# Kernel optimization log

Measured on AMD Instinct MI355X. Metric: run time of the kernel, lower is better.

The kernel has to match this reference:

```python
import jax, jax.numpy as jnp
import numpy as np

D = 512
B, S1, S2 = 8, 2048, 2048


def setup_inputs() -> dict:
    key = jax.random.key(0)
    ks = jax.random.split(key, 8)
    s = 1.0 / np.sqrt(D)
    return {
        "x1": jax.random.normal(ks[0], (B, S1, D), dtype=jnp.float32),
        "x2": jax.random.normal(ks[1], (B, S2, D), dtype=jnp.float32),
        "Wq": jax.random.normal(ks[2], (D, D), dtype=jnp.float32) * s,
        "bq": jnp.zeros((D,), dtype=jnp.float32),
        "Wk": jax.random.normal(ks[3], (D, D), dtype=jnp.float32) * s,
        "bk": jnp.zeros((D,), dtype=jnp.float32),
        "Wv": jax.random.normal(ks[4], (D, D), dtype=jnp.float32) * s,
        "bv": jnp.zeros((D,), dtype=jnp.float32),
    }


def reference(x1, x2, Wq, bq, Wk, bk, Wv, bv):
    # q,k,v projections (torch Linear: x @ W^T + b)
    q = jnp.einsum("bsd,ed->bse", x1, Wq) + bq  # [B,S1,D]
    k = jnp.einsum("btd,ed->bte", x2, Wk) + bk  # [B,S2,D]
    v = jnp.einsum("btd,ed->bte", x2, Wv) + bv  # [B,S2,D]
    # NOTE: source scales by input_dim (D), not sqrt(D)
    scores = jnp.einsum("bse,bte->bst", q, k) / D  # [B,S1,S2]
    attn = jax.nn.softmax(scores, axis=-1)
    return jnp.einsum("bst,bte->bse", attn, v)  # [B,S1,D]
```

## Files before the change

### kernel.cpp

```cpp
#include <hip/hip_runtime.h>

using u16 = unsigned short;
using u32 = unsigned int;
using s16x8 = __attribute__((ext_vector_type(8))) short;
using bf16x8 = __attribute__((ext_vector_type(8))) __bf16;
using f32x4 = __attribute__((ext_vector_type(4))) float;

__device__ inline u16 f2bf(float f) {
  u32 u = __float_as_uint(f);
  u = (u + 0x7FFFu + ((u >> 16) & 1u)) >> 16;
  return (u16)u;
}

__device__ inline f32x4 mfma16(s16x8 a, s16x8 b, f32x4 c) {
  return __builtin_amdgcn_mfma_f32_16x16x32_bf16(
      __builtin_bit_cast(bf16x8, a), __builtin_bit_cast(bf16x8, b), c, 0, 0, 0);
}

__device__ inline void load_lds16(const void* g, void* l) {
  __builtin_amdgcn_global_load_lds(
      (const __attribute__((address_space(1))) void*)g,
      (__attribute__((address_space(3))) void*)l, 16, 0, 0);
}

__global__ __launch_bounds__(256) void cast_x12(
    const float* __restrict__ x1, const float* __restrict__ x2,
    u16* __restrict__ o1, u16* __restrict__ o2) {
  const float* in = blockIdx.y ? x2 : x1;
  u16* out = blockIdx.y ? o2 : o1;
  int i = (blockIdx.x * 256 + threadIdx.x) * 4;
  float4 f = *(const float4*)(in + i);
  ushort4 o;
  o.x = f2bf(f.x); o.y = f2bf(f.y); o.z = f2bf(f.z); o.w = f2bf(f.w);
  *(ushort4*)(out + i) = o;
}

__global__ __launch_bounds__(256) void cast_w3z(
    const float* __restrict__ a, const float* __restrict__ b,
    const float* __restrict__ c, u16* __restrict__ oa, u16* __restrict__ ob,
    u16* __restrict__ oc, float* __restrict__ lbuf) {
  if (blockIdx.y == 3) {
    if (blockIdx.x < 64) lbuf[blockIdx.x * 256 + threadIdx.x] = 0.0f;
    return;
  }
  const float* in = blockIdx.y == 0 ? a : (blockIdx.y == 1 ? b : c);
  u16* out = blockIdx.y == 0 ? oa : (blockIdx.y == 1 ? ob : oc);
  int i = (blockIdx.x * 256 + threadIdx.x) * 4;
  float4 f = *(const float4*)(in + i);
  ushort4 o;
  o.x = f2bf(f.x); o.y = f2bf(f.y); o.z = f2bf(f.z); o.w = f2bf(f.w);
  *(ushort4*)(out + i) = o;
}

template <int EPI>
__global__ __launch_bounds__(256) void gemm64(
    const u16* __restrict__ A, const u16* __restrict__ B,
    const u16* __restrict__ B2, void* __restrict__ C, void* __restrict__ C2,
    const float* __restrict__ bias, const float* __restrict__ bias2,
    float* __restrict__ lsum, float scale,
    int M, int N, int K, long sA, long sB, long sC) {
  const int bz = blockIdx.z;
  const int m0 = blockIdx.y * 128;
  const int n0 = blockIdx.x * 128;
  const u16* Ab = A + (size_t)bz * sA;
  const u16* Bsel = (EPI == 4 && n0 >= 512) ? B2 : B;
  const int nb = (EPI == 4 && n0 >= 512) ? n0 - 512 : n0;
  const u16* Bb = Bsel + (size_t)bz * sB;
  const int tid = threadIdx.x;
  const int lane = tid & 63;
  const int wave = tid >> 6;
  const int wm = (wave >> 1) * 64;
  const int wn = (wave & 1) * 64;

  __shared__ u16 SM[128 * 64 * 2];
  u16* As = SM;
  u16* Bs = SM + 128 * 64;

  const int sr = lane >> 3;
  const int gd = (lane & 7) ^ sr;
  const int ch0 = wave * 4;

  f32x4 acc[4][4];
#pragma unroll
  for (int i = 0; i < 4; ++i)
#pragma unroll
    for (int j = 0; j < 4; ++j) acc[i][j] = 0.0f;

  const int fr = lane & 15;
  const int fg = lane >> 4;

  for (int k0 = 0; k0 < K; k0 += 64) {
#pragma unroll
    for (int it = 0; it < 4; ++it) {
      const int ch = ch0 + it;
      const int row = ch * 8 + sr;
      load_lds16(Ab + (size_t)(m0 + row) * K + k0 + gd * 8, &As[ch * 512]);
      load_lds16(Bb + (size_t)(nb + row) * K + k0 + gd * 8, &Bs[ch * 512]);
    }
    __syncthreads();
#pragma unroll
    for (int s = 0; s < 2; ++s) {
      const int slot = ((s * 4 + fg) ^ (fr & 7)) * 8;
      s16x8 af[4], bfr[4];
#pragma unroll
      for (int i = 0; i < 4; ++i) {
        af[i]  = *(const s16x8*)&As[(wm + i * 16 + fr) * 64 + slot];
        bfr[i] = *(const s16x8*)&Bs[(wn + i * 16 + fr) * 64 + slot];
      }
#pragma unroll
      for (int mi = 0; mi < 4; ++mi)
#pragma unroll
        for (int ni = 0; ni < 4; ++ni)
          acc[mi][ni] = mfma16(af[mi], bfr[ni], acc[mi][ni]);
    }
    __syncthreads();
  }

  const int er = fg * 4;
  const int ec = fr;

  if (EPI == 0) {
    u16* Cb = (u16*)C;
#pragma unroll
    for (int mi = 0; mi < 4; ++mi)
#pragma unroll
      for (int ni = 0; ni < 4; ++ni) {
        const int col = n0 + wn + ni * 16 + ec;
        const float badd = bias[col];
#pragma unroll
        for (int i = 0; i < 4; ++i) {
          const int row = m0 + wm + mi * 16 + er + i;
          Cb[(size_t)row * N + col] = f2bf(acc[mi][ni][i] + badd);
        }
      }
  } else if (EPI == 4) {
    if (n0 < 512) {
      u16* Cb = (u16*)C;
#pragma unroll
      for (int mi = 0; mi < 4; ++mi)
#pragma unroll
        for (int ni = 0; ni < 4; ++ni) {
          const int col = n0 + wn + ni * 16 + ec;
          const float badd = bias[col];
#pragma unroll
          for (int i = 0; i < 4; ++i) {
            const int row = m0 + wm + mi * 16 + er + i;
            Cb[(size_t)row * 512 + col] = f2bf(acc[mi][ni][i] + badd);
          }
        }
    } else {
      u16* Tb = SM;
      const int batch = m0 >> 11;
      const int srow = m0 & 2047;
      u16* Cv = (u16*)C2 + (size_t)batch * (512 * 2048);
#pragma unroll
      for (int h = 0; h < 2; ++h) {
        if ((wn >> 6) == h) {
#pragma unroll
          for (int mi = 0; mi < 4; ++mi)
#pragma unroll
            for (int ni = 0; ni < 4; ++ni) {
              const int c = ni * 16 + ec;
              const float badd = bias2[n0 - 512 + wn + c];
#pragma unroll
              for (int i = 0; i < 4; ++i) {
                const int r = wm + mi * 16 + er + i;
                Tb[c * 136 + r] = f2bf(acc[mi][ni][i] + badd);
              }
            }
        }
        __syncthreads();
        const int d = tid >> 2;
        const int sc = (tid & 3) * 32;
        const int dglob = n0 - 512 + 64 * h + d;
#pragma unroll
        for (int j = 0; j < 4; ++j) {
          uint4 v = *(const uint4*)&Tb[d * 136 + sc + j * 8];
          *(uint4*)&Cv[(size_t)dglob * 2048 + srow + sc + j * 8] = v;
        }
        __syncthreads();
      }
    }
  } else if (EPI == 2) {
    u16* Cb = (u16*)C + (size_t)bz * sC;
#pragma unroll
    for (int mi = 0; mi < 4; ++mi) {
      float rs[4] = {0.0f, 0.0f, 0.0f, 0.0f};
#pragma unroll
      for (int ni = 0; ni < 4; ++ni) {
        const int col = n0 + wn + ni * 16 + ec;
#pragma unroll
        for (int i = 0; i < 4; ++i) {
          const float p = __expf(acc[mi][ni][i] * scale);
          rs[i] += p;
          Cb[(size_t)(m0 + wm + mi * 16 + er + i) * N + col] = f2bf(p);
        }
      }
#pragma unroll
      for (int i = 0; i < 4; ++i) {
        rs[i] += __shfl_xor(rs[i], 1);
        rs[i] += __shfl_xor(rs[i], 2);
        rs[i] += __shfl_xor(rs[i], 4);
        rs[i] += __shfl_xor(rs[i], 8);
      }
      if (ec == 0) {
#pragma unroll
        for (int i = 0; i < 4; ++i)
          atomicAdd(&lsum[(size_t)bz * M + m0 + wm + mi * 16 + er + i], rs[i]);
      }
    }
  } else {
    float* Cb = (float*)C + (size_t)bz * sC;
#pragma unroll
    for (int mi = 0; mi < 4; ++mi)
#pragma unroll
      for (int i = 0; i < 4; ++i) {
        const int row = m0 + wm + mi * 16 + er + i;
        const float li = __builtin_amdgcn_rcpf(lsum[(size_t)bz * M + row]);
#pragma unroll
        for (int ni = 0; ni < 4; ++ni) {
          const int col = n0 + wn + ni * 16 + ec;
          Cb[(size_t)row * N + col] = acc[mi][ni][i] * li;
        }
      }
  }
}

extern "C" void kernel_launch(void* const* d_in, const int* in_sizes, int n_in,
                              void* d_out, int out_size, void* d_ws, size_t ws_size,
                              hipStream_t stream) {
  constexpr int B = 8, S = 2048, D = 512;
  constexpr size_t MS = (size_t)B * S;

  const float* x1 = (const float*)d_in[0];
  const float* x2 = (const float*)d_in[1];
  const float* Wq = (const float*)d_in[2];
  const float* bq = (const float*)d_in[3];
  const float* Wk = (const float*)d_in[4];
  const float* bk = (const float*)d_in[5];
  const float* Wv = (const float*)d_in[6];
  const float* bv = (const float*)d_in[7];
  float* out = (float*)d_out;

  u16* x1b = (u16*)d_ws;
  u16* x2b = x1b + MS * D;
  u16* Wqb = x2b + MS * D;
  u16* Wkb = Wqb + (size_t)D * D;
  u16* Wvb = Wkb + (size_t)D * D;
  u16* qb  = Wvb + (size_t)D * D;
  u16* kb  = qb + MS * D;
  u16* vTb = kb + MS * D;
  u16* Sc  = vTb + MS * D;
  float* lbuf = (float*)(Sc + (size_t)B * S * S);

  dim3 blk(256);

  cast_x12<<<dim3((MS * D) / 1024, 2), blk, 0, stream>>>(x1, x2, x1b, x2b);
  cast_w3z<<<dim3((D * D) / 1024, 4), blk, 0, stream>>>(
      Wq, Wk, Wv, Wqb, Wkb, Wvb, lbuf);

  gemm64<0><<<dim3(4, 128, 1), blk, 0, stream>>>(
      x1b, Wqb, nullptr, qb, nullptr, bq, nullptr, nullptr, 0.0f,
      16384, 512, 512, 0, 0, 0);

  gemm64<4><<<dim3(8, 128, 1), blk, 0, stream>>>(
      x2b, Wkb, Wvb, kb, vTb, bk, bv, nullptr, 0.0f,
      16384, 512, 512, 0, 0, 0);

  gemm64<2><<<dim3(16, 16, B), blk, 0, stream>>>(
      qb, kb, nullptr, Sc, nullptr, nullptr, nullptr, lbuf, 1.0f / (float)D,
      2048, 2048, 512, (long)S * D, (long)S * D, (long)S * S);

  gemm64<3><<<dim3(4, 16, B), blk, 0, stream>>>(
      Sc, vTb, nullptr, out, nullptr, nullptr, nullptr, lbuf, 0.0f,
      2048, 512, 2048, (long)S * S, (long)D * S, (long)S * D);
}
```

Measured before the change: 291.2 us.

## Quantize Q and K to FP8 and use scaled FP8 MFMA for scores

```diff
diff --git a/kernel.cpp b/kernel.cpp
--- a/kernel.cpp
+++ b/kernel.cpp
@@ -1,10 +1,13 @@
 #include <hip/hip_runtime.h>
 
+using u8  = unsigned char;
 using u16 = unsigned short;
 using u32 = unsigned int;
 using s16x8 = __attribute__((ext_vector_type(8))) short;
 using bf16x8 = __attribute__((ext_vector_type(8))) __bf16;
 using f32x4 = __attribute__((ext_vector_type(4))) float;
+using i32x4 = __attribute__((ext_vector_type(4))) int;
+using i32x8 = __attribute__((ext_vector_type(8))) int;
 
 __device__ inline u16 f2bf(float f) {
   u32 u = __float_as_uint(f);
@@ -12,9 +15,18 @@
   return (u16)u;
 }
 
+__device__ inline u8 f2fp8(float f) {
+  return (u8)(__builtin_amdgcn_cvt_pk_fp8_f32(f, f, 0, false) & 0xFF);
+}
+
 __device__ inline f32x4 mfma16(s16x8 a, s16x8 b, f32x4 c) {
   return __builtin_amdgcn_mfma_f32_16x16x32_bf16(
       __builtin_bit_cast(bf16x8, a), __builtin_bit_cast(bf16x8, b), c, 0, 0, 0);
+}
+
+__device__ inline f32x4 mfma_fp8(i32x8 a, i32x8 b, f32x4 c) {
+  return __builtin_amdgcn_mfma_scale_f32_16x16x128_f8f6f4(
+      a, b, c, 0 , 0 , 0, 127, 0, 127);
 }
 
 __device__ inline void load_lds16(const void* g, void* l) {
@@ -57,7 +69,7 @@
     const u16* __restrict__ A, const u16* __restrict__ B,
     const u16* __restrict__ B2, void* __restrict__ C, void* __restrict__ C2,
     const float* __restrict__ bias, const float* __restrict__ bias2,
-    float* __restrict__ lsum, float scale,
+    const float* __restrict__ lsum,
     int M, int N, int K, long sA, long sB, long sC) {
   const int bz = blockIdx.z;
   const int m0 = blockIdx.y * 128;
@@ -120,7 +132,7 @@
   const int ec = fr;
 
   if (EPI == 0) {
-    u16* Cb = (u16*)C;
+    u8* Cb = (u8*)C;
 #pragma unroll
     for (int mi = 0; mi < 4; ++mi)
 #pragma unroll
@@ -130,12 +142,12 @@
 #pragma unroll
         for (int i = 0; i < 4; ++i) {
           const int row = m0 + wm + mi * 16 + er + i;
-          Cb[(size_t)row * N + col] = f2bf(acc[mi][ni][i] + badd);
+          Cb[(size_t)row * N + col] = f2fp8(acc[mi][ni][i] + badd);
         }
       }
   } else if (EPI == 4) {
     if (n0 < 512) {
-      u16* Cb = (u16*)C;
+      u8* Cb = (u8*)C;
 #pragma unroll
       for (int mi = 0; mi < 4; ++mi)
 #pragma unroll
@@ -145,7 +157,7 @@
 #pragma unroll
           for (int i = 0; i < 4; ++i) {
             const int row = m0 + wm + mi * 16 + er + i;
-            Cb[(size_t)row * 512 + col] = f2bf(acc[mi][ni][i] + badd);
+            Cb[(size_t)row * 512 + col] = f2fp8(acc[mi][ni][i] + badd);
           }
         }
     } else {
@@ -181,34 +193,6 @@
         __syncthreads();
       }
     }
-  } else if (EPI == 2) {
-    u16* Cb = (u16*)C + (size_t)bz * sC;
-#pragma unroll
-    for (int mi = 0; mi < 4; ++mi) {
-      float rs[4] = {0.0f, 0.0f, 0.0f, 0.0f};
-#pragma unroll
-      for (int ni = 0; ni < 4; ++ni) {
-        const int col = n0 + wn + ni * 16 + ec;
-#pragma unroll
-        for (int i = 0; i < 4; ++i) {
-          const float p = __expf(acc[mi][ni][i] * scale);
-          rs[i] += p;
-          Cb[(size_t)(m0 + wm + mi * 16 + er + i) * N + col] = f2bf(p);
-        }
-      }
-#pragma unroll
-      for (int i = 0; i < 4; ++i) {
-        rs[i] += __shfl_xor(rs[i], 1);
-        rs[i] += __shfl_xor(rs[i], 2);
-        rs[i] += __shfl_xor(rs[i], 4);
-        rs[i] += __shfl_xor(rs[i], 8);
-      }
-      if (ec == 0) {
-#pragma unroll
-        for (int i = 0; i < 4; ++i)
-          atomicAdd(&lsum[(size_t)bz * M + m0 + wm + mi * 16 + er + i], rs[i]);
-      }
-    }
   } else {
     float* Cb = (float*)C + (size_t)bz * sC;
 #pragma unroll
@@ -223,6 +207,102 @@
           Cb[(size_t)row * N + col] = acc[mi][ni][i] * li;
         }
       }
+  }
+}
+
+__global__ __launch_bounds__(256) void gemm_fp8_scores(
+    const u8* __restrict__ A, const u8* __restrict__ B, u16* __restrict__ C,
+    float* __restrict__ lsum, float scale,
+    int M, int N, int K, long sA, long sB, long sC) {
+  const int bz = blockIdx.z;
+  const int m0 = blockIdx.y * 128;
+  const int n0 = blockIdx.x * 128;
+  const u8* Ab = A + (size_t)bz * sA;
+  const u8* Bb = B + (size_t)bz * sB;
+  const int tid = threadIdx.x;
+  const int lane = tid & 63;
+  const int wave = tid >> 6;
+  const int wm = (wave >> 1) * 64;
+  const int wn = (wave & 1) * 64;
+
+  __shared__ u8 As8[128 * 128];
+  __shared__ u8 Bs8[128 * 128];
+
+  const int sr = lane >> 3;
+  const int gd = (lane & 7) ^ sr;
+  const int ch0 = wave * 4;
+
+  f32x4 acc[4][4];
+#pragma unroll
+  for (int i = 0; i < 4; ++i)
+#pragma unroll
+    for (int j = 0; j < 4; ++j) acc[i][j] = 0.0f;
+
+  const int fr = lane & 15;
+  const int fg = lane >> 4;
+  const int r7 = fr & 7;
+  const int s0 = (2 * fg) ^ r7;
+  const int s1 = s0 ^ 1;
+
+  for (int k0 = 0; k0 < K; k0 += 128) {
+#pragma unroll
+    for (int it = 0; it < 4; ++it) {
+      const int ch = ch0 + it;
+      const int row = ch * 8 + sr;
+      load_lds16(Ab + (size_t)(m0 + row) * K + k0 + gd * 16, &As8[ch * 1024]);
+      load_lds16(Bb + (size_t)(n0 + row) * K + k0 + gd * 16, &Bs8[ch * 1024]);
+    }
+    __syncthreads();
+    i32x8 af[4], bfv[4];
+#pragma unroll
+    for (int i = 0; i < 4; ++i) {
+      const u8* pa = &As8[(wm + i * 16 + fr) * 128];
+      i32x4 alo = *(const i32x4*)(pa + s0 * 16);
+      i32x4 ahi = *(const i32x4*)(pa + s1 * 16);
+      af[i][0] = alo[0]; af[i][1] = alo[1]; af[i][2] = alo[2]; af[i][3] = alo[3];
+      af[i][4] = ahi[0]; af[i][5] = ahi[1]; af[i][6] = ahi[2]; af[i][7] = ahi[3];
+      const u8* pb = &Bs8[(wn + i * 16 + fr) * 128];
+      i32x4 blo = *(const i32x4*)(pb + s0 * 16);
+      i32x4 bhi = *(const i32x4*)(pb + s1 * 16);
+      bfv[i][0] = blo[0]; bfv[i][1] = blo[1]; bfv[i][2] = blo[2]; bfv[i][3] = blo[3];
+      bfv[i][4] = bhi[0]; bfv[i][5] = bhi[1]; bfv[i][6] = bhi[2]; bfv[i][7] = bhi[3];
+    }
+#pragma unroll
+    for (int mi = 0; mi < 4; ++mi)
+#pragma unroll
+      for (int ni = 0; ni < 4; ++ni)
+        acc[mi][ni] = mfma_fp8(af[mi], bfv[ni], acc[mi][ni]);
+    __syncthreads();
+  }
+
+  const int er = fg * 4;
+  const int ec = fr;
+  u16* Cb = C + (size_t)bz * sC;
+#pragma unroll
+  for (int mi = 0; mi < 4; ++mi) {
+    float rs[4] = {0.0f, 0.0f, 0.0f, 0.0f};
+#pragma unroll
+    for (int ni = 0; ni < 4; ++ni) {
+      const int col = n0 + wn + ni * 16 + ec;
+#pragma unroll
+      for (int i = 0; i < 4; ++i) {
+        const float p = __expf(acc[mi][ni][i] * scale);
+        rs[i] += p;
+        Cb[(size_t)(m0 + wm + mi * 16 + er + i) * N + col] = f2bf(p);
+      }
+    }
+#pragma unroll
+    for (int i = 0; i < 4; ++i) {
+      rs[i] += __shfl_xor(rs[i], 1);
+      rs[i] += __shfl_xor(rs[i], 2);
+      rs[i] += __shfl_xor(rs[i], 4);
+      rs[i] += __shfl_xor(rs[i], 8);
+    }
+    if (ec == 0) {
+#pragma unroll
+      for (int i = 0; i < 4; ++i)
+        atomicAdd(&lsum[(size_t)bz * M + m0 + wm + mi * 16 + er + i], rs[i]);
+    }
   }
 }
 
@@ -247,11 +327,11 @@
   u16* Wqb = x2b + MS * D;
   u16* Wkb = Wqb + (size_t)D * D;
   u16* Wvb = Wkb + (size_t)D * D;
-  u16* qb  = Wvb + (size_t)D * D;
-  u16* kb  = qb + MS * D;
-  u16* vTb = kb + MS * D;
+  u16* vTb = Wvb + (size_t)D * D;
   u16* Sc  = vTb + MS * D;
   float* lbuf = (float*)(Sc + (size_t)B * S * S);
+  u8* qb8 = (u8*)(lbuf + MS);
+  u8* kb8 = qb8 + MS * D;
 
   dim3 blk(256);
 
@@ -260,18 +340,18 @@
       Wq, Wk, Wv, Wqb, Wkb, Wvb, lbuf);
 
   gemm64<0><<<dim3(4, 128, 1), blk, 0, stream>>>(
-      x1b, Wqb, nullptr, qb, nullptr, bq, nullptr, nullptr, 0.0f,
+      x1b, Wqb, nullptr, qb8, nullptr, bq, nullptr, nullptr,
       16384, 512, 512, 0, 0, 0);
 
   gemm64<4><<<dim3(8, 128, 1), blk, 0, stream>>>(
-      x2b, Wkb, Wvb, kb, vTb, bk, bv, nullptr, 0.0f,
+      x2b, Wkb, Wvb, kb8, vTb, bk, bv, nullptr,
       16384, 512, 512, 0, 0, 0);
 
-  gemm64<2><<<dim3(16, 16, B), blk, 0, stream>>>(
-      qb, kb, nullptr, Sc, nullptr, nullptr, nullptr, lbuf, 1.0f / (float)D,
-      2048, 2048, 512, (long)S * D, (long)S * D, (long)S * S);
+  gemm_fp8_scores<<<dim3(16, 16, B), blk, 0, stream>>>(
+      qb8, kb8, Sc, lbuf, 1.0f / (float)D, 2048, 2048, 512,
+      (long)S * D, (long)S * D, (long)S * S);
 
   gemm64<3><<<dim3(4, 16, B), blk, 0, stream>>>(
-      Sc, vTb, nullptr, out, nullptr, nullptr, nullptr, lbuf, 0.0f,
+      Sc, vTb, nullptr, out, nullptr, nullptr, nullptr, lbuf,
       2048, 512, 2048, (long)S * S, (long)D * S, (long)S * D);
 }
```

New measurement: 259.3 us. 11.0% less time.
